# Performance work log

Hardware: AMD Instinct MI355X
Metric: run time of the kernel (lower is better)

Reference implementation:

```python
import jax, jax.numpy as jnp
import numpy as np

B, N, C = 4, 262144, 10
K_PRE, K_POST = 4096, 500          # before_nms_max, after_nms_max
ROI_THR, NMS_THR = 0.1, 0.01       # roi_threshold, nms_threshold


def setup_inputs() -> dict:
    key = jax.random.key(0)
    k1, k2, k3, k4 = jax.random.split(key, 4)
    # raw logits; sigmoid(-2 + noise) straddles roi_threshold=0.1 realistically
    cls = jax.random.normal(k1, (B, N, C), jnp.float32) - 2.0
    centers = jax.random.uniform(k2, (B, N, 3), jnp.float32, minval=-50.0, maxval=50.0)
    sizes = jax.random.uniform(k3, (B, N, 3), jnp.float32, minval=0.5, maxval=5.0)
    heading = jax.random.uniform(k4, (B, N, 1), jnp.float32, minval=-np.pi, maxval=np.pi)
    boxes = jnp.concatenate([centers, sizes, heading], axis=-1)  # (B, N, 7)
    return {"batch_cls_preds": cls, "batch_box_preds": boxes}


def _pairwise_bev_iou(b):
    # b: (K, 7) = [x, y, z, dx, dy, dz, heading]; BEV IoU (heading ignored,
    # axis-aligned approximation of the rotated-IoU CUDA kernel).
    x, y, dx, dy = b[:, 0], b[:, 1], b[:, 3], b[:, 4]
    x1, x2 = x - dx * 0.5, x + dx * 0.5
    y1, y2 = y - dy * 0.5, y + dy * 0.5
    ix = jnp.clip(jnp.minimum(x2[:, None], x2[None, :]) - jnp.maximum(x1[:, None], x1[None, :]), 0.0)
    iy = jnp.clip(jnp.minimum(y2[:, None], y2[None, :]) - jnp.maximum(y1[:, None], y1[None, :]), 0.0)
    inter = ix * iy                              # (K, K)
    area = dx * dy                               # (K,)
    union = area[:, None] + area[None, :] - inter
    return inter / jnp.maximum(union, 1e-6)


def _nms_one(scores, labels, boxes):
    # scores: (N,), labels: (N,) int32, boxes: (N, 7)
    s = jnp.where(scores > ROI_THR, scores, -1.0)       # score-threshold filter
    topv, topi = jax.lax.top_k(s, K_PRE)                # keep top before_nms_max
    tb = boxes[topi]                                     # (K_PRE, 7)
    tl = labels[topi]
    iou = _pairwise_bev_iou(tb)                          # (K_PRE, K_PRE)
    keep0 = topv > ROI_THR

    def body(i, keep):
        # a kept higher-score box i suppresses later boxes with IoU > thr
        sup = (iou[i] > NMS_THR) & (jnp.arange(K_PRE) > i) & keep[i]
        return keep & ~sup

    keep = jax.lax.fori_loop(0, K_PRE, body, keep0)
    kept_scores = jnp.where(keep, topv, -1.0)
    fv, fi = jax.lax.top_k(kept_scores, K_POST)          # after_nms_max slots
    m = fv > 0.0
    final_scores = jnp.where(m, fv, 0.0)                 # (K_POST,)
    final_boxes = tb[fi] * m[:, None].astype(tb.dtype)   # (K_POST, 7)
    final_labels = jnp.where(m, tl[fi], -1)              # (K_POST,)
    return final_scores, final_boxes, final_labels


def reference(batch_cls_preds, batch_box_preds):
    probs = jax.nn.sigmoid(batch_cls_preds)              # (B, N, C)
    scores = jnp.max(probs, axis=-1)                     # per-anchor best class score
    labels = jnp.argmax(probs, axis=-1).astype(jnp.int32)
    final_scores, final_boxes, final_labels = jax.vmap(_nms_one)(scores, labels, batch_box_preds)
    return final_scores, final_boxes, final_labels
```

## Files before the change

kernel.cpp:

```cpp
#include <hip/hip_runtime.h>
#include <stdint.h>

constexpr int B = 4;
constexpr int N = 262144;
constexpr int C = 10;
constexpr int KPRE = 4096;
constexpr int KPOST = 500;
constexpr float ROI_THR = 0.1f;
constexpr float NMS_THR = 0.01f;
constexpr int CAP = 8192;
constexpr int MASKW = KPRE / 64;
constexpr int RJT = 2;

__device__ __forceinline__ uint32_t f2k(float f) {
  uint32_t u = __float_as_uint(f);
  return (u & 0x80000000u) ? ~u : (u | 0x80000000u);
}
__device__ __forceinline__ float k2f(uint32_t k) {
  uint32_t u = (k & 0x80000000u) ? (k ^ 0x80000000u) : ~k;
  return __uint_as_float(u);
}
__device__ __forceinline__ float sigm(float x) { return 1.0f / (1.0f + expf(-x)); }

__device__ __forceinline__ void async_lds16(const void* g, void* l) {
  __builtin_amdgcn_global_load_lds((const __attribute__((address_space(1))) void*)g,
                                   (__attribute__((address_space(3))) void*)l, 16, 0, 0);
}

__device__ __forceinline__ uint2 select256(const uint32_t* __restrict__ h, uint32_t R,
                                           uint32_t* s, uint32_t* o2) {
  int t = threadIdx.x;
  s[t] = h[t];
  __syncthreads();
  for (int off = 1; off < 256; off <<= 1) {
    uint32_t v = s[t] + ((t + off < 256) ? s[t + off] : 0u);
    __syncthreads();
    s[t] = v;
    __syncthreads();
  }
  uint32_t suf = s[t];
  uint32_t sufn = (t < 255) ? s[t + 1] : 0u;
  if (suf >= R && R > sufn) {
    o2[0] = (uint32_t)t;
    o2[1] = R - sufn;
  }
  __syncthreads();
  uint2 r;
  r.x = o2[0];
  r.y = o2[1];
  __syncthreads();
  return r;
}

__global__ void scoreK(const float* __restrict__ cls, uint32_t* __restrict__ keys,
                       uint32_t* __restrict__ hist0) {
  __shared__ float ls[2560];
  __shared__ uint32_t h[256];
  int b = blockIdx.y;
  int t = threadIdx.x;
  h[t] = 0;
  size_t base = ((size_t)b * N + (size_t)blockIdx.x * 256) * C;
  const float2* g2 = (const float2*)(cls + base);
  float2* l2 = (float2*)ls;
#pragma unroll
  for (int r = 0; r < 5; ++r) l2[r * 256 + t] = g2[r * 256 + t];
  __syncthreads();
  const float* mine = ls + t * 10;
  float m = mine[0];
#pragma unroll
  for (int c = 1; c < C; ++c) m = fmaxf(m, mine[c]);
  float p = sigm(m);
  float sc = (p > ROI_THR) ? p : -1.0f;
  uint32_t k = f2k(sc);
  keys[(size_t)b * N + blockIdx.x * 256 + t] = k;
  atomicAdd(&h[k >> 24], 1u);
  __syncthreads();
  if (h[t]) atomicAdd(&hist0[b * 256 + t], h[t]);
}

__global__ void histP1K(const uint32_t* __restrict__ keys, const uint32_t* __restrict__ hist0,
                        uint32_t* __restrict__ hist1) {
  __shared__ uint32_t s[256];
  __shared__ uint32_t o2[2];
  __shared__ uint32_t h[256];
  int b = blockIdx.y;
  int t = threadIdx.x;
  uint2 s0 = select256(hist0 + b * 256, (uint32_t)KPRE, s, o2);
  h[t] = 0;
  __syncthreads();
  uint32_t pref = s0.x;
  const uint4* kb4 = (const uint4*)(keys + (size_t)b * N);
#pragma unroll
  for (int r = 0; r < 2; ++r) {
    uint4 kv = kb4[blockIdx.x * 512 + r * 256 + t];
#pragma unroll
    for (int j = 0; j < 4; ++j) {
      uint32_t k = (&kv.x)[j];
      if ((k >> 24) == pref) atomicAdd(&h[(k >> 16) & 255u], 1u);
    }
  }
  __syncthreads();
  if (h[t]) atomicAdd(&hist1[b * 256 + t], h[t]);
}

__global__ void compactK(const uint32_t* __restrict__ keys, const uint32_t* __restrict__ hist0,
                         const uint32_t* __restrict__ hist1, unsigned long long* __restrict__ list,
                         uint32_t* __restrict__ cnt) {
  __shared__ uint32_t s[256];
  __shared__ uint32_t o2[2];
  __shared__ uint32_t scan[256];
  __shared__ uint32_t baseSh;
  int b = blockIdx.y;
  int t = threadIdx.x;
  uint2 s0 = select256(hist0 + b * 256, (uint32_t)KPRE, s, o2);
  uint2 s1 = select256(hist1 + b * 256, s0.y, s, o2);
  uint32_t T = ((s0.x << 8) | s1.x) << 16;
  const uint4* kb4 = (const uint4*)(keys + (size_t)b * N);
  uint4 kv[4];
#pragma unroll
  for (int r = 0; r < 4; ++r) kv[r] = kb4[blockIdx.x * 1024 + r * 256 + t];
  uint32_t c = 0;
#pragma unroll
  for (int r = 0; r < 4; ++r)
#pragma unroll
    for (int j = 0; j < 4; ++j) c += ((&kv[r].x)[j] >= T) ? 1u : 0u;
  scan[t] = c;
  __syncthreads();
  for (int off = 1; off < 256; off <<= 1) {
    uint32_t v = scan[t] + ((t >= off) ? scan[t - off] : 0u);
    __syncthreads();
    scan[t] = v;
    __syncthreads();
  }
  uint32_t excl = scan[t] - c;
  if (t == 255) baseSh = atomicAdd(&cnt[b], scan[255]);
  __syncthreads();
  uint32_t pos = baseSh + excl;
#pragma unroll
  for (int r = 0; r < 4; ++r)
#pragma unroll
    for (int j = 0; j < 4; ++j) {
      uint32_t k = (&kv[r].x)[j];
      if (k >= T) {
        uint32_t n = (blockIdx.x * 1024 + r * 256 + t) * 4 + j;
        if (pos < CAP)
          list[(size_t)b * CAP + pos] = ((unsigned long long)k << 32) | (uint32_t)(~n);
        pos++;
      }
    }
}

__global__ void rankK(const unsigned long long* __restrict__ list, const uint32_t* __restrict__ cnt,
                      uint32_t* __restrict__ rank) {
  __shared__ unsigned long long lp[256];
  int b = blockIdx.z;
  int cc = (int)min(cnt[b], (uint32_t)CAP);
  if (blockIdx.x * 256 >= cc) return;
  int j0 = blockIdx.y * (256 * RJT);
  if (j0 >= cc) return;
  int i = blockIdx.x * 256 + threadIdx.x;
  unsigned long long pi = (i < cc) ? list[(size_t)b * CAP + i] : ~0ull;
  uint32_t c = 0;
#pragma unroll
  for (int tb = 0; tb < RJT; ++tb) {
    int j = j0 + tb * 256 + threadIdx.x;
    __syncthreads();
    lp[threadIdx.x] = (j < cc) ? list[(size_t)b * CAP + j] : 0ull;
    __syncthreads();
#pragma unroll 8
    for (int jj = 0; jj < 256; ++jj) c += (lp[jj] > pi) ? 1u : 0u;
  }
  if (i < cc && c) atomicAdd(&rank[(size_t)b * CAP + i], c);
}

__global__ void scatterK(const unsigned long long* __restrict__ list,
                         const uint32_t* __restrict__ cnt, const uint32_t* __restrict__ rank,
                         const float* __restrict__ boxes, float* __restrict__ sel_score,
                         uint32_t* __restrict__ sel_idx, float* __restrict__ sel_box) {
  int b = blockIdx.y;
  int p = blockIdx.x * 256 + threadIdx.x;
  uint32_t cc = min(cnt[b], (uint32_t)CAP);
  if (p >= (int)cc) return;
  unsigned long long pk = list[(size_t)b * CAP + p];
  uint32_t r = rank[(size_t)b * CAP + p];
  if (r >= (uint32_t)KPRE) return;
  uint32_t key = (uint32_t)(pk >> 32);
  uint32_t idx = ~(uint32_t)pk;
  sel_score[b * KPRE + r] = k2f(key);
  sel_idx[b * KPRE + r] = idx;
  const float* src = boxes + ((size_t)b * N + idx) * 7;
  float* dst = sel_box + ((size_t)b * KPRE + r) * 8;
#pragma unroll
  for (int c = 0; c < 7; ++c) dst[c] = src[c];
  dst[7] = 0.f;
}

__global__ void maskK(const float* __restrict__ sel_box, unsigned long long* __restrict__ mask) {
  int b = blockIdx.z;
  int bi = blockIdx.x;
  int w = blockIdx.y;
  int t = threadIdx.x;
  int i = bi * 256 + t;
  int j0 = w * 64;
  unsigned long long* dst = mask + ((size_t)b * KPRE + i) * MASKW + w;
  if (j0 + 63 <= bi * 256) {
    *dst = 0ull;
    return;
  }
  __shared__ float4 jv[64];
  __shared__ float ja[64];
  if (t < 64) {
    const float4* bj = (const float4*)(sel_box + ((size_t)b * KPRE + j0 + t) * 8);
    float4 lo = bj[0], hi = bj[1];
    float xj = lo.x, yj = lo.y, dxj = lo.w, dyj = hi.x;
    float hxj = __fmul_rn(dxj, 0.5f), hyj = __fmul_rn(dyj, 0.5f);
    float4 v;
    v.x = __fsub_rn(xj, hxj);
    v.y = __fadd_rn(xj, hxj);
    v.z = __fsub_rn(yj, hyj);
    v.w = __fadd_rn(yj, hyj);
    jv[t] = v;
    ja[t] = __fmul_rn(dxj, dyj);
  }
  __syncthreads();
  const float4* myb = (const float4*)(sel_box + ((size_t)b * KPRE + i) * 8);
  float4 lo = myb[0], hi = myb[1];
  float x = lo.x, y = lo.y, dx = lo.w, dy = hi.x;
  float hx = __fmul_rn(dx, 0.5f), hy = __fmul_rn(dy, 0.5f);
  float x1i = __fsub_rn(x, hx), x2i = __fadd_rn(x, hx);
  float y1i = __fsub_rn(y, hy), y2i = __fadd_rn(y, hy);
  float ai = __fmul_rn(dx, dy);
  unsigned long long wacc = 0ull;
#pragma unroll 16
  for (int jj = 0; jj < 64; ++jj) {
    int j = j0 + jj;
    float4 v = jv[jj];
    float aj = ja[jj];
    float xx1 = fmaxf(x1i, v.x);
    float xx2 = fminf(x2i, v.y);
    float yy1 = fmaxf(y1i, v.z);
    float yy2 = fminf(y2i, v.w);
    float ix = fmaxf(__fsub_rn(xx2, xx1), 0.0f);
    float iy = fmaxf(__fsub_rn(yy2, yy1), 0.0f);
    float inter = __fmul_rn(ix, iy);
    float den = fmaxf(__fsub_rn(__fadd_rn(ai, aj), inter), 1e-6f);
    float q0 = __fmul_rn(NMS_THR, den);
    float d = __fsub_rn(inter, q0);
    bool sup = d > 0.0f;
    if (__builtin_expect(__any(fabsf(d) <= q0 * 1e-5f), 0)) {
      sup = (inter / den) > NMS_THR;
    }
    sup = sup && (j > i);
    wacc |= ((unsigned long long)(sup ? 1u : 0u)) << jj;
  }
  *dst = wacc;
}

__global__ void nmsK(const unsigned long long* __restrict__ mask,
                     const float* __restrict__ sel_score,
                     uint32_t* __restrict__ kept_pos, uint32_t* __restrict__ kept_cnt) {
  __shared__ unsigned long long lds[2][64][64];
  int b = blockIdx.x;
  int t = threadIdx.x;

  unsigned long long cand = 0ull;
  for (int k = 0; k < 64; ++k) {
    float s = sel_score[b * KPRE + k * 64 + t];
    unsigned long long bal = __ballot(s > ROI_THR);
    if (t == k) cand = bal;
  }

  const unsigned long long* mb = mask + (size_t)b * KPRE * MASKW;
  unsigned long long remv = 0ull;
  int kc = 0;

  auto prefetch = [&](int g, int buf2) {
    const char* base = (const char*)(mb + (size_t)g * 64 * MASKW);
#pragma unroll
    for (int p = 0; p < 32; ++p)
      async_lds16(base + (size_t)p * 1024 + (size_t)t * 16, &lds[buf2][p * 2][0]);
  };

  prefetch(0, 0);
  for (int g = 0; g < 64; ++g) {
    int buf = g & 1;
    asm volatile("s_waitcnt vmcnt(0)" ::: "memory");
    if (g + 1 < 64) prefetch(g + 1, buf ^ 1);

    unsigned long long cw = cand & ~remv;
    unsigned long long aw = (unsigned long long)__shfl((long long)cw, g, 64);
    if (aw) {
      unsigned long long m = lds[buf][t][g];
      unsigned long long K = __ballot((m & aw) != 0ull);
      unsigned long long alive = aw;
      unsigned long long rem = aw & K;
      if (rem) {
        bool deadf = ((aw >> t) & 1ull) == 0ull;
        while (rem) {
          int s = __ffsll((long long)rem) - 1;
          rem &= rem - 1ull;
          if ((alive >> s) & 1ull) {
            unsigned long long row_s = lds[buf][s][g];
            deadf = deadf || (((row_s >> t) & 1ull) != 0ull);
            alive = __ballot(!deadf);
            rem &= alive;
          }
        }
      }
      int grp = __popcll(alive);
      if ((alive >> t) & 1ull) {
        int rk = __popcll(alive & ((1ull << t) - 1ull));
        if (kc + rk < KPOST) kept_pos[b * KPOST + kc + rk] = g * 64 + t;
      }
      unsigned long long acc = 0ull, a2 = alive;
      while (a2) {
        int s2 = __ffsll((long long)a2) - 1;
        a2 &= a2 - 1ull;
        acc |= lds[buf][s2][t];
      }
      remv |= acc;
      kc += grp;
      if (kc >= KPOST) break;
    }
  }
  asm volatile("s_waitcnt vmcnt(0)" ::: "memory");
  if (t == 0) kept_cnt[b] = (uint32_t)min(kc, KPOST);
}

__global__ void outK(const float* __restrict__ cls,
                     const float* __restrict__ sel_score, const uint32_t* __restrict__ sel_idx,
                     const float* __restrict__ sel_box,
                     const uint32_t* __restrict__ kept_pos, const uint32_t* __restrict__ kept_cnt,
                     float* __restrict__ out) {
  int b = blockIdx.y;
  int s = blockIdx.x * blockDim.x + threadIdx.x;
  if (s >= KPOST) return;
  float* oS = out;
  float* oB = out + B * KPOST;
  float* oL = out + B * KPOST + B * KPOST * 7;
  uint32_t kcnt = kept_cnt[b];
  if (s < (int)kcnt) {
    uint32_t pos = kept_pos[b * KPOST + s];
    oS[b * KPOST + s] = sel_score[b * KPRE + pos];
    const float* box = sel_box + ((size_t)b * KPRE + pos) * 8;
    float* dst = oB + ((size_t)b * KPOST + s) * 7;
#pragma unroll
    for (int c = 0; c < 7; ++c) dst[c] = box[c];
    uint32_t idx = sel_idx[b * KPRE + pos];
    const float* p = cls + ((size_t)b * N + idx) * C;
    float bestv = sigm(p[0]);
    int bestc = 0;
#pragma unroll
    for (int c = 1; c < C; ++c) {
      float v = sigm(p[c]);
      if (v > bestv) { bestv = v; bestc = c; }
    }
    oL[b * KPOST + s] = (float)bestc;
  } else {
    oS[b * KPOST + s] = 0.0f;
    float* dst = oB + ((size_t)b * KPOST + s) * 7;
#pragma unroll
    for (int c = 0; c < 7; ++c) dst[c] = 0.0f;
    oL[b * KPOST + s] = -1.0f;
  }
}

__global__ void sentinelK(float* out, int n) {
  int i = blockIdx.x * blockDim.x + threadIdx.x;
  if (i < n) out[i] = 1337.0f;
}

extern "C" void kernel_launch(void* const* d_in, const int* in_sizes, int n_in,
                              void* d_out, int out_size, void* d_ws, size_t ws_size,
                              hipStream_t stream) {
  const float* cls = (const float*)d_in[0];
  const float* boxes = (const float*)d_in[1];
  float* out = (float*)d_out;

  char* ws = (char*)d_ws;
  size_t off = 0;
  auto alloc = [&](size_t bytes) -> void* {
    void* p = ws + off;
    off = (off + bytes + 255) & ~(size_t)255;
    return p;
  };
  unsigned long long* mask = (unsigned long long*)alloc((size_t)B * KPRE * MASKW * 8);
  unsigned long long* list = (unsigned long long*)alloc((size_t)B * CAP * 8);
  uint32_t* keys = (uint32_t*)alloc((size_t)B * N * 4);
  float* sel_box = (float*)alloc((size_t)B * KPRE * 8 * 4);
  float* sel_score = (float*)alloc((size_t)B * KPRE * 4);
  uint32_t* sel_idx = (uint32_t*)alloc((size_t)B * KPRE * 4);
  uint32_t* kept_pos = (uint32_t*)alloc((size_t)B * KPOST * 4);
  uint32_t* kept_cnt = (uint32_t*)alloc(B * 4);

  uint32_t* hist0 = (uint32_t*)mask;
  uint32_t* hist1 = hist0 + B * 256;
  uint32_t* cnt = hist1 + B * 256;
  uint32_t* rank = (uint32_t*)((char*)mask + 16384);
  size_t zbytes = 16384 + (size_t)B * CAP * 4;

  if (off > ws_size) {
    sentinelK<<<dim3((out_size + 255) / 256), 256, 0, stream>>>(out, out_size);
    return;
  }

  hipMemsetAsync(mask, 0, zbytes, stream);
  scoreK<<<dim3(N / 256, B), 256, 0, stream>>>(cls, keys, hist0);
  histP1K<<<dim3(N / 2048, B), 256, 0, stream>>>(keys, hist0, hist1);
  compactK<<<dim3(N / 4096, B), 256, 0, stream>>>(keys, hist0, hist1, list, cnt);
  rankK<<<dim3(CAP / 256, CAP / (256 * RJT), B), 256, 0, stream>>>(list, cnt, rank);
  scatterK<<<dim3(CAP / 256, B), 256, 0, stream>>>(list, cnt, rank, boxes, sel_score, sel_idx,
                                                   sel_box);
  maskK<<<dim3(16, 64, B), 256, 0, stream>>>(sel_box, mask);
  nmsK<<<B, 64, 0, stream>>>(mask, sel_score, kept_pos, kept_cnt);
  outK<<<dim3((KPOST + 255) / 256, B), 256, 0, stream>>>(cls, sel_score, sel_idx, sel_box,
                                                         kept_pos, kept_cnt, out);
}
```

Before: 154.0 us.

## Precompute transposed diagonal mask blocks and deepen NMS prefetch to two groups

Adds a kernel that transposes each 64x64 diagonal block of the suppression mask with ballots, so the serial NMS loop reads its own column from a register instead of doing a dependent LDS load for each suppressor. The NMS kernel now prefetches two groups ahead with a partial vmcnt wait, which keeps more global-to-LDS traffic in flight during the serial scan. The cost is one extra small kernel launch and a workspace buffer, plus tighter reliance on exact waitcnt accounting.

After: 161.9 us. +5.1%, slower.

```diff
diff --git a/kernel.cpp b/kernel.cpp
--- a/kernel.cpp
+++ b/kernel.cpp
@@ -256,10 +256,27 @@
   *dst = wacc;
 }
 
+__global__ void transK(const unsigned long long* __restrict__ mask,
+                       unsigned long long* __restrict__ Tmat) {
+  int b = blockIdx.y;
+  int g = blockIdx.x;
+  int t = threadIdx.x;
+  unsigned long long m = mask[((size_t)b * KPRE + g * 64 + t) * MASKW + g];
+  unsigned long long T = 0ull;
+#pragma unroll
+  for (int j = 0; j < 64; ++j) {
+    unsigned long long bj = __ballot(((m >> j) & 1ull) != 0ull);
+    if (t == j) T = bj;
+  }
+  Tmat[((size_t)b * 64 + g) * 128 + t] = T;
+}
+
 __global__ void nmsK(const unsigned long long* __restrict__ mask,
+                     const unsigned long long* __restrict__ Tmat,
                      const float* __restrict__ sel_score,
                      uint32_t* __restrict__ kept_pos, uint32_t* __restrict__ kept_cnt) {
   __shared__ unsigned long long lds[2][64][64];
+  __shared__ unsigned long long tl[2][128];
   int b = blockIdx.x;
   int t = threadIdx.x;
 
@@ -271,26 +288,29 @@
   }
 
   const unsigned long long* mb = mask + (size_t)b * KPRE * MASKW;
+  const unsigned long long* tb = Tmat + (size_t)b * 64 * 128;
   unsigned long long remv = 0ull;
   int kc = 0;
 
-  auto prefetch = [&](int g, int buf2) {
-    const char* base = (const char*)(mb + (size_t)g * 64 * MASKW);
+  auto prefetch = [&](int g2, int buf2) {
+    const char* base = (const char*)(mb + (size_t)g2 * 64 * MASKW);
 #pragma unroll
     for (int p = 0; p < 32; ++p)
       async_lds16(base + (size_t)p * 1024 + (size_t)t * 16, &lds[buf2][p * 2][0]);
+    async_lds16((const char*)(tb + (size_t)g2 * 128) + (size_t)t * 16, &tl[buf2][0]);
   };
 
   prefetch(0, 0);
+  prefetch(1, 1);
   for (int g = 0; g < 64; ++g) {
     int buf = g & 1;
-    asm volatile("s_waitcnt vmcnt(0)" ::: "memory");
-    if (g + 1 < 64) prefetch(g + 1, buf ^ 1);
+    asm volatile("s_waitcnt vmcnt(33)" ::: "memory");
 
     unsigned long long cw = cand & ~remv;
     unsigned long long aw = (unsigned long long)__shfl((long long)cw, g, 64);
     if (aw) {
       unsigned long long m = lds[buf][t][g];
+      unsigned long long T = tl[buf][t];
       unsigned long long K = __ballot((m & aw) != 0ull);
       unsigned long long alive = aw;
       unsigned long long rem = aw & K;
@@ -300,8 +320,7 @@
           int s = __ffsll((long long)rem) - 1;
           rem &= rem - 1ull;
           if ((alive >> s) & 1ull) {
-            unsigned long long row_s = lds[buf][s][g];
-            deadf = deadf || (((row_s >> t) & 1ull) != 0ull);
+            deadf = deadf || (((T >> s) & 1ull) != 0ull);
             alive = __ballot(!deadf);
             rem &= alive;
           }
@@ -322,6 +341,10 @@
       kc += grp;
       if (kc >= KPOST) break;
     }
+    if (g + 2 < 64) {
+      asm volatile("s_waitcnt lgkmcnt(0)" ::: "memory");
+      prefetch(g + 2, buf);
+    }
   }
   asm volatile("s_waitcnt vmcnt(0)" ::: "memory");
   if (t == 0) kept_cnt[b] = (uint32_t)min(kc, KPOST);
@@ -392,6 +415,7 @@
   uint32_t* sel_idx = (uint32_t*)alloc((size_t)B * KPRE * 4);
   uint32_t* kept_pos = (uint32_t*)alloc((size_t)B * KPOST * 4);
   uint32_t* kept_cnt = (uint32_t*)alloc(B * 4);
+  unsigned long long* Tmat = (unsigned long long*)alloc((size_t)B * 64 * 128 * 8);
 
   uint32_t* hist0 = (uint32_t*)mask;
   uint32_t* hist1 = hist0 + B * 256;
@@ -412,7 +436,8 @@
   scatterK<<<dim3(CAP / 256, B), 256, 0, stream>>>(list, cnt, rank, boxes, sel_score, sel_idx,
                                                    sel_box);
   maskK<<<dim3(16, 64, B), 256, 0, stream>>>(sel_box, mask);
-  nmsK<<<B, 64, 0, stream>>>(mask, sel_score, kept_pos, kept_cnt);
+  transK<<<dim3(64, B), 64, 0, stream>>>(mask, Tmat);
+  nmsK<<<B, 64, 0, stream>>>(mask, Tmat, sel_score, kept_pos, kept_cnt);
   outK<<<dim3((KPOST + 255) / 256, B), 256, 0, stream>>>(cls, sel_score, sel_idx, sel_box,
                                                          kept_pos, kept_cnt, out);
 }
```
